# Optimization experiments

Hardware: AMD Instinct MI355X
Metric: run time of the kernel (lower is better)

## Reference

```python
import jax, jax.numpy as jnp
import numpy as np

B, N, D, H = 4, 2048, 512, 8
HD = D // H  # 64


def setup_inputs() -> dict:
    key = jax.random.key(0)
    ks = jax.random.split(key, 12)
    s = 0.02
    return {
        "x": jax.random.normal(ks[0], (B, N, D), jnp.float32),
        "freqs": jax.random.normal(ks[1], (B, N, HD // 2), jnp.float32),
        # weights stored as (in, out); torch Linear applies x @ W.T + b
        "wqkv_w": jax.random.normal(ks[2], (D, 3 * D), jnp.float32) * s,
        "wqkv_b": jax.random.normal(ks[3], (3 * D,), jnp.float32) * s,
        "out_w": jax.random.normal(ks[4], (D, D), jnp.float32) * s,
        "out_b": jax.random.normal(ks[5], (D,), jnp.float32) * s,
        "ffn1_w": jax.random.normal(ks[6], (2 * D, 2 * D), jnp.float32) * s,
        "ffn1_b": jax.random.normal(ks[7], (2 * D,), jnp.float32) * s,
        "ln_g": jnp.ones((2 * D,), jnp.float32),
        "ln_b": jnp.zeros((2 * D,), jnp.float32),
        "ffn2_w": jax.random.normal(ks[8], (2 * D, D), jnp.float32) * s,
        "ffn2_b": jax.random.normal(ks[9], (D,), jnp.float32) * s,
    }


def _rope(t, cos, sin):
    # t: [B,H,N,HD]; cos/sin: [B,1,N,HD/2]
    x1, x2 = t[..., ::2], t[..., 1::2]
    return jnp.stack([x1 * cos - x2 * sin, x1 * sin + x2 * cos], axis=-1).reshape(t.shape)


def reference(x, freqs, wqkv_w, wqkv_b, out_w, out_b,
              ffn1_w, ffn1_b, ln_g, ln_b, ffn2_w, ffn2_b):
    b, n, d = x.shape
    h, hd = H, d // H
    qkv = x @ wqkv_w + wqkv_b                      # [B,N,3D]
    q, k, v = jnp.split(qkv, 3, axis=-1)
    to_heads = lambda t: t.reshape(b, n, h, hd).transpose(0, 2, 1, 3)  # [B,H,N,HD]
    q, k, v = to_heads(q), to_heads(k), to_heads(v)
    cos = jnp.cos(freqs)[:, None]                  # [B,1,N,HD/2]
    sin = jnp.sin(freqs)[:, None]
    q = _rope(q, cos, sin)
    k = _rope(k, cos, sin)
    scale = hd ** -0.5
    attn = jax.nn.softmax(jnp.einsum('bhqd,bhkd->bhqk', q, k) * scale, axis=-1)
    msg = jnp.einsum('bhqk,bhkd->bhqd', attn, v).transpose(0, 2, 1, 3).reshape(b, n, d)
    msg = msg @ out_w + out_b
    # FFN on concat([x, msg]): Linear -> LayerNorm -> GELU(exact) -> Linear
    hcat = jnp.concatenate([x, msg], axis=-1) @ ffn1_w + ffn1_b   # [B,N,2D]
    mu = hcat.mean(-1, keepdims=True)
    var = hcat.var(-1, keepdims=True)
    hcat = (hcat - mu) * jax.lax.rsqrt(var + 1e-5) * ln_g + ln_b
    hcat = jax.nn.gelu(hcat, approximate=False)
    return x + hcat @ ffn2_w + ffn2_b
```

## Files before the change

### kernel.cpp

```cpp
#include <hip/hip_runtime.h>
#include <hip/hip_bf16.h>
#include <math.h>

typedef __bf16 bf16;
typedef __bf16 bf16x2 __attribute__((ext_vector_type(2)));
typedef __bf16 bf16x4 __attribute__((ext_vector_type(4)));
typedef __bf16 bf16x8 __attribute__((ext_vector_type(8)));
typedef float f32x4 __attribute__((ext_vector_type(4)));
typedef float f32x16 __attribute__((ext_vector_type(16)));

#define MFMA16(a, b, c) __builtin_amdgcn_mfma_f32_16x16x32_bf16(a, b, c, 0, 0, 0)
#define MFMA32(a, b, c) __builtin_amdgcn_mfma_f32_32x32x16_bf16(a, b, c, 0, 0, 0)


__global__ __launch_bounds__(256) void prep_kernel(
    const float* __restrict__ wqkv_w, const float* __restrict__ out_w,
    const float* __restrict__ ffn1_w, const float* __restrict__ ffn2_w,
    const float* __restrict__ x, const float* __restrict__ freqs,
    const float* __restrict__ ffn1_b, const float* __restrict__ out_b,
    bf16* __restrict__ wqkv_t, bf16* __restrict__ ffn2_t,
    bf16* __restrict__ fused_t, bf16* __restrict__ ffn1bt,
    bf16* __restrict__ out_cast, bf16* __restrict__ cat,
    float* __restrict__ bias_f, unsigned* __restrict__ tab)
{
    const int bid = blockIdx.x, tid = threadIdx.x;
    __shared__ bf16 tile[32][33];
    __shared__ float red[256];
    if (bid >= 6672) {
        int i = (bid - 6672) * 1024 + tid * 4;
        const float4 f = *(const float4*)(&freqs[i]);
        float s0, c0, s1, c1, s2, c2, s3, c3;
        __sincosf(f.x, &s0, &c0); __sincosf(f.y, &s1, &c1);
        __sincosf(f.z, &s2, &c2); __sincosf(f.w, &s3, &c3);
        union { bf16x2 h2; unsigned u; } p0, p1, p2, p3;
        p0.h2[0] = (bf16)c0; p0.h2[1] = (bf16)s0;
        p1.h2[0] = (bf16)c1; p1.h2[1] = (bf16)s1;
        p2.h2[0] = (bf16)c2; p2.h2[1] = (bf16)s2;
        p3.h2[0] = (bf16)c3; p3.h2[1] = (bf16)s3;
        uint4 o = {p0.u, p1.u, p2.u, p3.u};
        *(uint4*)(&tab[i]) = o;
        return;
    }
    if (bid >= 6656) {
        const int n = (bid - 6656) * 64 + (tid & 63);
        const int ic = tid >> 6;
        float acc = 0.f;
#pragma unroll 8
        for (int i = ic * 128; i < ic * 128 + 128; i++)
            acc += out_b[i] * ffn1_w[(size_t)(512 + i) * 1024 + n];
        red[tid] = acc;
        __syncthreads();
        if (tid < 64)
            bias_f[n] = ffn1_b[n] + red[tid] + red[tid + 64] + red[tid + 128] + red[tid + 192];
        return;
    }
    if (bid >= 2560) {
        int i = (bid - 2560) * 256 + tid;
        int row = i >> 7, col = (i & 127) << 2;
        const float4 v = *(const float4*)(&x[(size_t)row * 512 + col]);
        bf16x4 o; o[0] = (bf16)v.x; o[1] = (bf16)v.y; o[2] = (bf16)v.z; o[3] = (bf16)v.w;
        *(bf16x4*)(&cat[(size_t)row * 1024 + col]) = o;
        return;
    }
    if (bid >= 2304) {
        int i = (bid - 2304) * 1024 + tid * 4;
        const float4 v = *(const float4*)(&out_w[i]);
        bf16x4 o; o[0] = (bf16)v.x; o[1] = (bf16)v.y; o[2] = (bf16)v.z; o[3] = (bf16)v.w;
        *(bf16x4*)(&out_cast[i]) = o;
        return;
    }
    const float* src; bf16* dst; int C, ldd, bx, by;
    if (bid < 768)       { src = wqkv_w;            dst = wqkv_t;  C = 1536; ldd = 512;  int r = bid;        bx = r % 48; by = r / 48; }
    else if (bid < 1280) { src = ffn2_w;            dst = ffn2_t;  C = 512;  ldd = 1024; int r = bid - 768;  bx = r % 16; by = r / 16; }
    else if (bid < 1792) { src = ffn1_w;            dst = fused_t; C = 1024; ldd = 1024; int r = bid - 1280; bx = r % 32; by = r / 32; }
    else                 { src = ffn1_w + 512*1024; dst = ffn1bt;  C = 1024; ldd = 512;  int r = bid - 1792; bx = r % 32; by = r / 32; }
    const int tx = tid & 31, ty = tid >> 5;
    const int xx = bx * 32 + tx;
#pragma unroll
    for (int j = 0; j < 4; j++)
        tile[ty + 8 * j][tx] = (bf16)src[(size_t)(by * 32 + ty + 8 * j) * C + xx];
    __syncthreads();
    const int x2 = by * 32 + tx;
#pragma unroll
    for (int j = 0; j < 4; j++)
        dst[(size_t)(bx * 32 + ty + 8 * j) * ldd + x2] = tile[tx][ty + 8 * j];
}

__global__ __launch_bounds__(256) void qkv_wcomb_kernel(
    const bf16* __restrict__ cat, const bf16* __restrict__ wqkv_t,
    const float* __restrict__ wqkv_b, const unsigned* __restrict__ tab,
    bf16* __restrict__ qbuf, bf16* __restrict__ kbuf, bf16* __restrict__ vbuf,
    const bf16* __restrict__ ffn1bt, const bf16* __restrict__ out_cast,
    bf16* __restrict__ fused_t)
{
    const int bid = blockIdx.x;
    const bool isqkv = bid < 768;
    const bf16* A; const bf16* Bt; int lda, m0, n0;
    if (isqkv) { A = cat;    lda = 1024; Bt = wqkv_t;   n0 = (bid % 12) * 128; m0 = (bid / 12) * 128; }
    else       { int r = bid - 768;
                 A = ffn1bt; lda = 512;  Bt = out_cast; n0 = (r & 3) * 128;    m0 = (r >> 2) * 128; }
    const int K = 512;

    const int tid = threadIdx.x;
    const int lane = tid & 63, wave = tid >> 6;
    const int wm = wave >> 1, wn = wave & 1;
    const int l15 = lane & 15, quad = lane >> 4;

    __shared__ __align__(16) char smem[16384];
    bf16* As = (bf16*)smem;
    bf16* Bs = (bf16*)(smem + 8192);
    unsigned* tabs = (unsigned*)smem;

    const int c0 = tid, c1 = tid + 256;
    const int r0 = c0 >> 2, kc0 = (c0 & 3) << 3;
    const int r1 = c1 >> 2, kc1 = (c1 & 3) << 3;
    const bf16* pA0 = &A[(size_t)(m0 + r0) * lda + kc0];
    const bf16* pA1 = &A[(size_t)(m0 + r1) * lda + kc1];
    const bf16* pB0 = &Bt[(size_t)(n0 + r0) * K + kc0];
    const bf16* pB1 = &Bt[(size_t)(n0 + r1) * K + kc1];

    const f32x4 zero = {0.f, 0.f, 0.f, 0.f};
    f32x4 acc[4][4];
#pragma unroll
    for (int i = 0; i < 4; i++)
#pragma unroll
        for (int j = 0; j < 4; j++) acc[i][j] = zero;

    bf16x8 ra0 = *(const bf16x8*)pA0;
    bf16x8 ra1 = *(const bf16x8*)pA1;
    bf16x8 rb0 = *(const bf16x8*)pB0;
    bf16x8 rb1 = *(const bf16x8*)pB1;

    for (int k0 = 0; k0 < K; k0 += 32) {
        __syncthreads();
        *(bf16x8*)(&As[c0 * 8]) = ra0;
        *(bf16x8*)(&As[c1 * 8]) = ra1;
        *(bf16x8*)(&Bs[c0 * 8]) = rb0;
        *(bf16x8*)(&Bs[c1 * 8]) = rb1;
        __syncthreads();
        if (k0 + 32 < K) {
            ra0 = *(const bf16x8*)(pA0 + k0 + 32);
            ra1 = *(const bf16x8*)(pA1 + k0 + 32);
            rb0 = *(const bf16x8*)(pB0 + k0 + 32);
            rb1 = *(const bf16x8*)(pB1 + k0 + 32);
        }
        bf16x8 af[4], bfv[4];
#pragma unroll
        for (int t = 0; t < 4; t++) {
            af[t]  = *(const bf16x8*)(&As[(wm * 64 + t * 16 + l15) * 32 + quad * 8]);
            bfv[t] = *(const bf16x8*)(&Bs[(wn * 64 + t * 16 + l15) * 32 + quad * 8]);
        }
#pragma unroll
        for (int mt = 0; mt < 4; mt++)
#pragma unroll
            for (int nt = 0; nt < 4; nt++)
                acc[mt][nt] = MFMA16(af[mt], bfv[nt], acc[mt][nt]);
    }

    const int row_base = m0 + wm * 64;
    const int col_base = n0 + wn * 64;

    if (isqkv) {
        const int sector = col_base >> 9;
        const bool dorope = sector < 2;
        if (dorope) {
            __syncthreads();
#pragma unroll
            for (int ps = 0; ps < 4; ps++) {
                int idx = ps * 1024 + tid * 4;
                *(uint4*)(&tabs[idx]) = *(const uint4*)(&tab[(size_t)m0 * 32 + idx]);
            }
            __syncthreads();
        }
        const float SCQ = 0.125f * 1.44269504089f;
        bf16* dstbase = (sector == 0) ? qbuf : (sector == 1 ? kbuf : vbuf);
#pragma unroll
        for (int nt = 0; nt < 4; nt++) {
            const int col = col_base + nt * 16 + l15;
            const int cq = col & 511;
            const int h = cq >> 6, hd = cq & 63;
            const float bv = wqkv_b[col];
            const int ihalf = hd >> 1;
            const bool odd = (hd & 1) != 0;
#pragma unroll
            for (int mt = 0; mt < 4; mt++) {
#pragma unroll
                for (int r = 0; r < 4; r++) {
                    const int mrow = row_base + mt * 16 + quad * 4 + r;
                    float v = acc[mt][nt][r] + bv;
                    float o = v;
                    if (dorope) {
                        float p = __shfl_xor(v, 1);
                        const int rl = wm * 64 + mt * 16 + quad * 4 + r;
                        union { unsigned u; bf16x2 h2; } t2;
                        t2.u = tabs[rl * 32 + ihalf];
                        float cs = t2.h2[0], sn = t2.h2[1];
                        o = odd ? (p * sn + v * cs) : (v * cs - p * sn);
                        if (sector == 0) o *= SCQ;
                    }
                    const int b = mrow >> 11, n = mrow & 2047;
                    dstbase[(((size_t)b * 8 + h) * 2048 + n) * 64 + hd] = (bf16)o;
                }
            }
        }
    } else {
#pragma unroll
        for (int nt = 0; nt < 4; nt++) {
            const int col = col_base + nt * 16 + l15;
#pragma unroll
            for (int mt = 0; mt < 4; mt++) {
#pragma unroll
                for (int r = 0; r < 4; r++) {
                    const int row = row_base + mt * 16 + quad * 4 + r;
                    fused_t[(size_t)row * 1024 + 512 + col] = (bf16)acc[mt][nt][r];
                }
            }
        }
    }
}

template <int MODE>
__global__ __launch_bounds__(256) void gemm_mfma(
    const bf16* __restrict__ A, int lda, const bf16* __restrict__ Bt,
    const float* __restrict__ bias, void* __restrict__ outv,
    const float* __restrict__ auxf, int K)
{
    const int tid = threadIdx.x;
    const int lane = tid & 63, wave = tid >> 6;
    const int wm = wave >> 1, wn = wave & 1;
    const int l15 = lane & 15, quad = lane >> 4;
    const int m0 = blockIdx.y * 128;
    const int n0 = blockIdx.x * 128;

    __shared__ bf16 As[128 * 32];
    __shared__ bf16 Bs[128 * 32];

    const int c0 = tid, c1 = tid + 256;
    const int r0 = c0 >> 2, kc0 = (c0 & 3) << 3;
    const int r1 = c1 >> 2, kc1 = (c1 & 3) << 3;
    const bf16* pA0 = &A[(size_t)(m0 + r0) * lda + kc0];
    const bf16* pA1 = &A[(size_t)(m0 + r1) * lda + kc1];
    const bf16* pB0 = &Bt[(size_t)(n0 + r0) * K + kc0];
    const bf16* pB1 = &Bt[(size_t)(n0 + r1) * K + kc1];

    const f32x4 zero = {0.f, 0.f, 0.f, 0.f};
    f32x4 acc[4][4];
#pragma unroll
    for (int i = 0; i < 4; i++)
#pragma unroll
        for (int j = 0; j < 4; j++) acc[i][j] = zero;

    bf16x8 ra0 = *(const bf16x8*)pA0;
    bf16x8 ra1 = *(const bf16x8*)pA1;
    bf16x8 rb0 = *(const bf16x8*)pB0;
    bf16x8 rb1 = *(const bf16x8*)pB1;

    for (int k0 = 0; k0 < K; k0 += 32) {
        __syncthreads();
        *(bf16x8*)(&As[c0 * 8]) = ra0;
        *(bf16x8*)(&As[c1 * 8]) = ra1;
        *(bf16x8*)(&Bs[c0 * 8]) = rb0;
        *(bf16x8*)(&Bs[c1 * 8]) = rb1;
        __syncthreads();
        if (k0 + 32 < K) {
            ra0 = *(const bf16x8*)(pA0 + k0 + 32);
            ra1 = *(const bf16x8*)(pA1 + k0 + 32);
            rb0 = *(const bf16x8*)(pB0 + k0 + 32);
            rb1 = *(const bf16x8*)(pB1 + k0 + 32);
        }
        bf16x8 af[4], bfv[4];
#pragma unroll
        for (int t = 0; t < 4; t++) {
            af[t]  = *(const bf16x8*)(&As[(wm * 64 + t * 16 + l15) * 32 + quad * 8]);
            bfv[t] = *(const bf16x8*)(&Bs[(wn * 64 + t * 16 + l15) * 32 + quad * 8]);
        }
#pragma unroll
        for (int mt = 0; mt < 4; mt++)
#pragma unroll
            for (int nt = 0; nt < 4; nt++)
                acc[mt][nt] = MFMA16(af[mt], bfv[nt], acc[mt][nt]);
    }

    const int row_base = m0 + wm * 64;
    const int col_base = n0 + wn * 64;
#pragma unroll
    for (int nt = 0; nt < 4; nt++) {
        const int col = col_base + nt * 16 + l15;
        const float bv = bias[col];
#pragma unroll
        for (int mt = 0; mt < 4; mt++) {
#pragma unroll
            for (int r = 0; r < 4; r++) {
                const int row = row_base + mt * 16 + quad * 4 + r;
                float v = acc[mt][nt][r] + bv;
                if constexpr (MODE == 2) {
                    ((bf16*)outv)[(size_t)row * 1024 + col] = (bf16)v;
                } else {
                    v += auxf[(size_t)row * 512 + col];
                    ((float*)outv)[(size_t)row * 512 + col] = v;
                }
            }
        }
    }
}

__global__ __launch_bounds__(512) void attn_kernel(const bf16* __restrict__ qb,
                                                   const bf16* __restrict__ kb,
                                                   const bf16* __restrict__ vb,
                                                   bf16* __restrict__ cat)
{
    __shared__ __align__(16) char smem[35840];
    bf16* Ks  = (bf16*)smem;
    bf16* Vts = (bf16*)(smem + 128 * 72 * 2);

    const int tid = threadIdx.x, lane = tid & 63, wave = tid >> 6;
    const int l31 = lane & 31, half = lane >> 5;
    const int qg = wave >> 2, kh = wave & 3;
    const int bh = blockIdx.x >> 5, qt = blockIdx.x & 31;
    const int b = bh >> 3, h = bh & 7;
    const size_t base = (size_t)bh * 2048 * 64;
    const int m0 = qt * 64 + qg * 32;

    bf16x8 aq[4];
#pragma unroll
    for (int k4 = 0; k4 < 4; k4++)
        aq[k4] = *(const bf16x8*)(&qb[base + (size_t)(m0 + l31) * 64 + k4 * 16 + half * 8]);

    f32x16 accO[2];
#pragma unroll
    for (int i = 0; i < 16; i++) { accO[0][i] = 0.f; accO[1][i] = 0.f; }
    float lsum = 0.f;

    int krow[2], kcol[2];
#pragma unroll
    for (int i = 0; i < 2; i++) { int c = tid + i * 512; krow[i] = c >> 3; kcol[i] = (c & 7) << 3; }
    const int vpr = tid & 63, vdg = tid >> 6;

    bf16x8 kreg[2], vr0, vr1;
    auto prefetch = [&](int key0) {
#pragma unroll
        for (int i = 0; i < 2; i++)
            kreg[i] = *(const bf16x8*)(&kb[base + (size_t)(key0 + krow[i]) * 64 + kcol[i]]);
        vr0 = *(const bf16x8*)(&vb[base + (size_t)(key0 + 2 * vpr) * 64 + vdg * 8]);
        vr1 = *(const bf16x8*)(&vb[base + (size_t)(key0 + 2 * vpr + 1) * 64 + vdg * 8]);
    };

    prefetch(0);
    const int ko = kh * 32;
    for (int kt = 0; kt < 16; kt++) {
        __syncthreads();
#pragma unroll
        for (int i = 0; i < 2; i++)
            *(bf16x8*)(&Ks[krow[i] * 72 + kcol[i]]) = kreg[i];
#pragma unroll
        for (int j = 0; j < 8; j++) {
            bf16x2 pr; pr[0] = vr0[j]; pr[1] = vr1[j];
            *(bf16x2*)(&Vts[(vdg * 8 + j) * 136 + 2 * vpr]) = pr;
        }
        __syncthreads();
        if (kt < 15) prefetch((kt + 1) * 128);

        f32x16 s;
#pragma unroll
        for (int i = 0; i < 16; i++) s[i] = 0.f;
#pragma unroll
        for (int k4 = 0; k4 < 4; k4++) {
            bf16x8 ak = *(const bf16x8*)(&Ks[(ko + l31) * 72 + k4 * 16 + half * 8]);
            s = MFMA32(ak, aq[k4], s);
        }
        float p[16];
#pragma unroll
        for (int r = 0; r < 16; r++) p[r] = __builtin_amdgcn_exp2f(s[r]);
        lsum += (((p[0] + p[1]) + (p[2] + p[3])) + ((p[4] + p[5]) + (p[6] + p[7])))
              + (((p[8] + p[9]) + (p[10] + p[11])) + ((p[12] + p[13]) + (p[14] + p[15])));
        unsigned pk[8];
#pragma unroll
        for (int i2 = 0; i2 < 8; i2++) {
            union { bf16x2 hh; unsigned u; } t;
            t.hh[0] = (bf16)p[2 * i2]; t.hh[1] = (bf16)p[2 * i2 + 1];
            pk[i2] = t.u;
        }
        const unsigned sa = half ? pk[0] : pk[2];
        const unsigned sb = half ? pk[1] : pk[3];
        const unsigned sc2 = half ? pk[4] : pk[6];
        const unsigned sd = half ? pk[5] : pk[7];
        const unsigned ra = (unsigned)__shfl_xor((int)sa, 32);
        const unsigned rb = (unsigned)__shfl_xor((int)sb, 32);
        const unsigned rc = (unsigned)__shfl_xor((int)sc2, 32);
        const unsigned rd = (unsigned)__shfl_xor((int)sd, 32);
        union { bf16x8 v; unsigned u[4]; } B0, B1;
        B0.u[0] = half ? ra : pk[0];
        B0.u[1] = half ? rb : pk[1];
        B0.u[2] = half ? pk[2] : ra;
        B0.u[3] = half ? pk[3] : rb;
        B1.u[0] = half ? rc : pk[4];
        B1.u[1] = half ? rd : pk[5];
        B1.u[2] = half ? pk[6] : rc;
        B1.u[3] = half ? pk[7] : rd;
#pragma unroll
        for (int dh = 0; dh < 2; dh++) {
            bf16x8 av0 = *(const bf16x8*)(&Vts[(dh * 32 + l31) * 136 + ko + half * 8]);
            bf16x8 av1 = *(const bf16x8*)(&Vts[(dh * 32 + l31) * 136 + ko + 16 + half * 8]);
            accO[dh] = MFMA32(av0, B0.v, accO[dh]);
            accO[dh] = MFMA32(av1, B1.v, accO[dh]);
        }
    }

    auto slotp = [&](int s) { return (float*)smem + ((s * 2 + qg) * 64 + lane) * 33; };
    __syncthreads();
    if (kh == 1 || kh == 3) {
        float* pr2 = slotp(kh >> 1);
#pragma unroll
        for (int dh = 0; dh < 2; dh++)
#pragma unroll
            for (int r = 0; r < 16; r++) pr2[dh * 16 + r] = accO[dh][r];
        pr2[32] = lsum;
    }
    __syncthreads();
    if (kh == 0 || kh == 2) {
        float* pr2 = slotp(kh >> 1);
#pragma unroll
        for (int dh = 0; dh < 2; dh++)
#pragma unroll
            for (int r = 0; r < 16; r++) accO[dh][r] += pr2[dh * 16 + r];
        lsum += pr2[32];
    }
    __syncthreads();
    if (kh == 2) {
        float* pr2 = slotp(0);
#pragma unroll
        for (int dh = 0; dh < 2; dh++)
#pragma unroll
            for (int r = 0; r < 16; r++) pr2[dh * 16 + r] = accO[dh][r];
        pr2[32] = lsum;
    }
    __syncthreads();
    if (kh == 0) {
        float* pr2 = slotp(0);
#pragma unroll
        for (int dh = 0; dh < 2; dh++)
#pragma unroll
            for (int r = 0; r < 16; r++) accO[dh][r] += pr2[dh * 16 + r];
        lsum += pr2[32];
        lsum += __shfl_xor(lsum, 32);
        const float inv = 1.0f / lsum;
        const int n = m0 + l31;
        bf16* aor = cat + ((size_t)b * 2048 + n) * 1024 + 512 + h * 64;
#pragma unroll
        for (int dh = 0; dh < 2; dh++) {
#pragma unroll
            for (int g = 0; g < 4; g++) {
                bf16x4 o4;
#pragma unroll
                for (int e = 0; e < 4; e++) o4[e] = (bf16)(accO[dh][g * 4 + e] * inv);
                *(bf16x4*)(&aor[dh * 32 + g * 8 + half * 4]) = o4;
            }
        }
    }
}

__global__ __launch_bounds__(256) void ln_gelu_kernel(bf16* __restrict__ hb,
                                                      const float* __restrict__ g,
                                                      const float* __restrict__ bt)
{
    const int row = blockIdx.x, tid = threadIdx.x;
    const int lane = tid & 63, wave = tid >> 6;
    bf16* hr = hb + (size_t)row * 1024;
    bf16x4 hv = *(const bf16x4*)(&hr[tid * 4]);
    float v0 = hv[0], v1 = hv[1], v2 = hv[2], v3 = hv[3];
    float s = v0 + v1 + v2 + v3;
    float q = v0 * v0 + v1 * v1 + v2 * v2 + v3 * v3;
    for (int o = 32; o; o >>= 1) { s += __shfl_xor(s, o); q += __shfl_xor(q, o); }
    __shared__ float red[8];
    if (lane == 0) { red[wave] = s; red[4 + wave] = q; }
    __syncthreads();
    s = red[0] + red[1] + red[2] + red[3];
    q = red[4] + red[5] + red[6] + red[7];
    const float mu = s * (1.f / 1024.f);
    const float rstd = rsqrtf(q * (1.f / 1024.f) - mu * mu + 1e-5f);
    const float4 gv = *(const float4*)(&g[tid * 4]);
    const float4 bv = *(const float4*)(&bt[tid * 4]);
    float vv[4] = {v0, v1, v2, v3};
    const float gg[4] = {gv.x, gv.y, gv.z, gv.w};
    const float bb[4] = {bv.x, bv.y, bv.z, bv.w};
    bf16x4 o4;
#pragma unroll
    for (int i = 0; i < 4; i++) {
        float y = (vv[i] - mu) * rstd * gg[i] + bb[i];
        float t = 1.5957691216f * y * (1.0f + 0.044715f * y * y);
        float e = __builtin_amdgcn_exp2f(-1.44269504089f * t);
        o4[i] = (bf16)(y * __builtin_amdgcn_rcpf(1.0f + e));
    }
    *(bf16x4*)(&hr[tid * 4]) = o4;
}

extern "C" void kernel_launch(void* const* d_in, const int* in_sizes, int n_in,
                              void* d_out, int out_size, void* d_ws, size_t ws_size,
                              hipStream_t stream) {
    (void)in_sizes; (void)n_in; (void)out_size; (void)ws_size;
    const float* x      = (const float*)d_in[0];
    const float* freqs  = (const float*)d_in[1];
    const float* wqkv_w = (const float*)d_in[2];
    const float* wqkv_b = (const float*)d_in[3];
    const float* out_w  = (const float*)d_in[4];
    const float* out_b  = (const float*)d_in[5];
    const float* ffn1_w = (const float*)d_in[6];
    const float* ffn1_b = (const float*)d_in[7];
    const float* ln_g   = (const float*)d_in[8];
    const float* ln_b   = (const float*)d_in[9];
    const float* ffn2_w = (const float*)d_in[10];
    const float* ffn2_b = (const float*)d_in[11];
    float* out = (float*)d_out;
    bf16* ws   = (bf16*)d_ws;

    bf16* wqkv_t   = ws;
    bf16* ffn2_t   = wqkv_t + 1536 * 512;
    bf16* fused_t  = ffn2_t + 512 * 1024;
    bf16* ffn1bt   = fused_t + 1024 * 1024;
    bf16* out_cast = ffn1bt + 1024 * 512;
    bf16* cat      = out_cast + 512 * 512;
    bf16* qbuf     = cat + (size_t)8192 * 1024;
    bf16* kbuf     = qbuf + (size_t)8192 * 512;
    bf16* vbuf     = kbuf + (size_t)8192 * 512;
    float* bias_f  = (float*)(vbuf + (size_t)8192 * 512);
    unsigned* tab  = (unsigned*)(bias_f + 1024);
    bf16* hbuf     = qbuf;

    prep_kernel<<<6928, 256, 0, stream>>>(wqkv_w, out_w, ffn1_w, ffn2_w, x, freqs,
                                          ffn1_b, out_b,
                                          wqkv_t, ffn2_t, fused_t, ffn1bt, out_cast, cat,
                                          bias_f, tab);
    qkv_wcomb_kernel<<<800, 256, 0, stream>>>(cat, wqkv_t, wqkv_b, tab, qbuf, kbuf, vbuf,
                                              ffn1bt, out_cast, fused_t);
    attn_kernel<<<1024, 512, 0, stream>>>(qbuf, kbuf, vbuf, cat);
    gemm_mfma<2><<<dim3(8, 64), 256, 0, stream>>>(cat, 1024, fused_t, bias_f, hbuf, nullptr, 1024);
    ln_gelu_kernel<<<8192, 256, 0, stream>>>(hbuf, ln_g, ln_b);
    gemm_mfma<3><<<dim3(4, 64), 256, 0, stream>>>(hbuf, 1024, ffn2_t, ffn2_b, out, x, 1024);
}
```

Before: 256.4 us.

## Software-pipeline attention PV with double-buffered V tile and shrink GEMM N tiles

The attention kernel double-buffers the transposed V tile in shared memory and defers each tile's P·V MFMAs to the next iteration, so they issue alongside the next QK^T and exp work. This is meant to hide MFMA and exp latency, at the cost of more LDS per block (which may lower occupancy). Separately, the FFN GEMMs switch from 128x128 to 128x64 tiles, doubling the grid for better CU fill on the 256-CU part in exchange for less B-operand reuse per block.

```diff
diff --git a/kernel.cpp b/kernel.cpp
--- a/kernel.cpp
+++ b/kernel.cpp
@@ -220,75 +220,71 @@
 }
 
 template <int MODE>
-__global__ __launch_bounds__(256) void gemm_mfma(
+__global__ __launch_bounds__(256) void gemm64_mfma(
     const bf16* __restrict__ A, int lda, const bf16* __restrict__ Bt,
     const float* __restrict__ bias, void* __restrict__ outv,
     const float* __restrict__ auxf, int K)
 {
     const int tid = threadIdx.x;
     const int lane = tid & 63, wave = tid >> 6;
-    const int wm = wave >> 1, wn = wave & 1;
     const int l15 = lane & 15, quad = lane >> 4;
     const int m0 = blockIdx.y * 128;
-    const int n0 = blockIdx.x * 128;
+    const int n0 = blockIdx.x * 64;
 
     __shared__ bf16 As[128 * 32];
-    __shared__ bf16 Bs[128 * 32];
+    __shared__ bf16 Bs[64 * 32];
 
     const int c0 = tid, c1 = tid + 256;
-    const int r0 = c0 >> 2, kc0 = (c0 & 3) << 3;
-    const int r1 = c1 >> 2, kc1 = (c1 & 3) << 3;
-    const bf16* pA0 = &A[(size_t)(m0 + r0) * lda + kc0];
-    const bf16* pA1 = &A[(size_t)(m0 + r1) * lda + kc1];
-    const bf16* pB0 = &Bt[(size_t)(n0 + r0) * K + kc0];
-    const bf16* pB1 = &Bt[(size_t)(n0 + r1) * K + kc1];
+    const int ar0 = c0 >> 2, akc0 = (c0 & 3) << 3;
+    const int ar1 = c1 >> 2, akc1 = (c1 & 3) << 3;
+    const int br0 = tid >> 2, bkc0 = (tid & 3) << 3;
+    const bf16* pA0 = &A[(size_t)(m0 + ar0) * lda + akc0];
+    const bf16* pA1 = &A[(size_t)(m0 + ar1) * lda + akc1];
+    const bf16* pB0 = &Bt[(size_t)(n0 + br0) * K + bkc0];
 
     const f32x4 zero = {0.f, 0.f, 0.f, 0.f};
-    f32x4 acc[4][4];
-#pragma unroll
-    for (int i = 0; i < 4; i++)
+    f32x4 acc[2][4];
+#pragma unroll
+    for (int i = 0; i < 2; i++)
 #pragma unroll
         for (int j = 0; j < 4; j++) acc[i][j] = zero;
 
     bf16x8 ra0 = *(const bf16x8*)pA0;
     bf16x8 ra1 = *(const bf16x8*)pA1;
     bf16x8 rb0 = *(const bf16x8*)pB0;
-    bf16x8 rb1 = *(const bf16x8*)pB1;
 
     for (int k0 = 0; k0 < K; k0 += 32) {
         __syncthreads();
         *(bf16x8*)(&As[c0 * 8]) = ra0;
         *(bf16x8*)(&As[c1 * 8]) = ra1;
-        *(bf16x8*)(&Bs[c0 * 8]) = rb0;
-        *(bf16x8*)(&Bs[c1 * 8]) = rb1;
+        *(bf16x8*)(&Bs[tid * 8]) = rb0;
         __syncthreads();
         if (k0 + 32 < K) {
             ra0 = *(const bf16x8*)(pA0 + k0 + 32);
             ra1 = *(const bf16x8*)(pA1 + k0 + 32);
             rb0 = *(const bf16x8*)(pB0 + k0 + 32);
-            rb1 = *(const bf16x8*)(pB1 + k0 + 32);
-        }
-        bf16x8 af[4], bfv[4];
-#pragma unroll
-        for (int t = 0; t < 4; t++) {
-            af[t]  = *(const bf16x8*)(&As[(wm * 64 + t * 16 + l15) * 32 + quad * 8]);
-            bfv[t] = *(const bf16x8*)(&Bs[(wn * 64 + t * 16 + l15) * 32 + quad * 8]);
-        }
-#pragma unroll
-        for (int mt = 0; mt < 4; mt++)
+        }
+        bf16x8 af[2], bfv[4];
+#pragma unroll
+        for (int t = 0; t < 2; t++)
+            af[t] = *(const bf16x8*)(&As[(wave * 32 + t * 16 + l15) * 32 + quad * 8]);
+#pragma unroll
+        for (int t = 0; t < 4; t++)
+            bfv[t] = *(const bf16x8*)(&Bs[(t * 16 + l15) * 32 + quad * 8]);
+#pragma unroll
+        for (int mt = 0; mt < 2; mt++)
 #pragma unroll
             for (int nt = 0; nt < 4; nt++)
                 acc[mt][nt] = MFMA16(af[mt], bfv[nt], acc[mt][nt]);
     }
 
-    const int row_base = m0 + wm * 64;
-    const int col_base = n0 + wn * 64;
+    const int row_base = m0 + wave * 32;
 #pragma unroll
     for (int nt = 0; nt < 4; nt++) {
-        const int col = col_base + nt * 16 + l15;
+        const int col = n0 + nt * 16 + l15;
         const float bv = bias[col];
 #pragma unroll
-        for (int mt = 0; mt < 4; mt++) {
+        for (int mt = 0; mt < 2; mt++) {
 #pragma unroll
             for (int r = 0; r < 4; r++) {
                 const int row = row_base + mt * 16 + quad * 4 + r;
@@ -309,9 +305,10 @@
                                                    const bf16* __restrict__ vb,
                                                    bf16* __restrict__ cat)
 {
-    __shared__ __align__(16) char smem[35840];
-    bf16* Ks  = (bf16*)smem;
-    bf16* Vts = (bf16*)(smem + 128 * 72 * 2);
+    __shared__ __align__(16) char smem[53248];
+    bf16* Ks   = (bf16*)smem;
+    bf16* Vts0 = (bf16*)(smem + 18432);
+    bf16* Vts1 = (bf16*)(smem + 35840);
 
     const int tid = threadIdx.x, lane = tid & 63, wave = tid >> 6;
     const int l31 = lane & 31, half = lane >> 5;
@@ -345,9 +342,24 @@
         vr1 = *(const bf16x8*)(&vb[base + (size_t)(key0 + 2 * vpr + 1) * 64 + vdg * 8]);
     };
 
+    const int ko = kh * 32;
+    union Bu { bf16x8 v; unsigned u[4]; };
+    Bu B0p, B1p;
+    auto pv = [&](const bf16* Vr) {
+#pragma unroll
+        for (int dh = 0; dh < 2; dh++) {
+            bf16x8 av0 = *(const bf16x8*)(&Vr[(dh * 32 + l31) * 136 + ko + half * 8]);
+            bf16x8 av1 = *(const bf16x8*)(&Vr[(dh * 32 + l31) * 136 + ko + 16 + half * 8]);
+            accO[dh] = MFMA32(av0, B0p.v, accO[dh]);
+            accO[dh] = MFMA32(av1, B1p.v, accO[dh]);
+        }
+    };
+
     prefetch(0);
-    const int ko = kh * 32;
+#pragma unroll
     for (int kt = 0; kt < 16; kt++) {
+        bf16* Vw = (kt & 1) ? Vts1 : Vts0;
+        bf16* Vr = (kt & 1) ? Vts0 : Vts1;
         __syncthreads();
 #pragma unroll
         for (int i = 0; i < 2; i++)
@@ -355,7 +367,7 @@
 #pragma unroll
         for (int j = 0; j < 8; j++) {
             bf16x2 pr; pr[0] = vr0[j]; pr[1] = vr1[j];
-            *(bf16x2*)(&Vts[(vdg * 8 + j) * 136 + 2 * vpr]) = pr;
+            *(bf16x2*)(&Vw[(vdg * 8 + j) * 136 + 2 * vpr]) = pr;
         }
         __syncthreads();
         if (kt < 15) prefetch((kt + 1) * 128);
@@ -368,6 +380,7 @@
             bf16x8 ak = *(const bf16x8*)(&Ks[(ko + l31) * 72 + k4 * 16 + half * 8]);
             s = MFMA32(ak, aq[k4], s);
         }
+        if (kt > 0) pv(Vr);
         float p[16];
 #pragma unroll
         for (int r = 0; r < 16; r++) p[r] = __builtin_amdgcn_exp2f(s[r]);
@@ -388,25 +401,18 @@
         const unsigned rb = (unsigned)__shfl_xor((int)sb, 32);
         const unsigned rc = (unsigned)__shfl_xor((int)sc2, 32);
         const unsigned rd = (unsigned)__shfl_xor((int)sd, 32);
-        union { bf16x8 v; unsigned u[4]; } B0, B1;
-        B0.u[0] = half ? ra : pk[0];
-        B0.u[1] = half ? rb : pk[1];
-        B0.u[2] = half ? pk[2] : ra;
-        B0.u[3] = half ? pk[3] : rb;
-        B1.u[0] = half ? rc : pk[4];
-        B1.u[1] = half ? rd : pk[5];
-        B1.u[2] = half ? pk[6] : rc;
-        B1.u[3] = half ? pk[7] : rd;
-#pragma unroll
-        for (int dh = 0; dh < 2; dh++) {
-            bf16x8 av0 = *(const bf16x8*)(&Vts[(dh * 32 + l31) * 136 + ko + half * 8]);
-            bf16x8 av1 = *(const bf16x8*)(&Vts[(dh * 32 + l31) * 136 + ko + 16 + half * 8]);
-            accO[dh] = MFMA32(av0, B0.v, accO[dh]);
-            accO[dh] = MFMA32(av1, B1.v, accO[dh]);
-        }
-    }
-
-    auto slotp = [&](int s) { return (float*)smem + ((s * 2 + qg) * 64 + lane) * 33; };
+        B0p.u[0] = half ? ra : pk[0];
+        B0p.u[1] = half ? rb : pk[1];
+        B0p.u[2] = half ? pk[2] : ra;
+        B0p.u[3] = half ? pk[3] : rb;
+        B1p.u[0] = half ? rc : pk[4];
+        B1p.u[1] = half ? rd : pk[5];
+        B1p.u[2] = half ? pk[6] : rc;
+        B1p.u[3] = half ? pk[7] : rd;
+    }
+    pv(Vts1);
+
+    auto slotp = [&](int s2) { return (float*)smem + ((s2 * 2 + qg) * 64 + lane) * 33; };
     __syncthreads();
     if (kh == 1 || kh == 3) {
         float* pr2 = slotp(kh >> 1);
@@ -533,7 +539,7 @@
     qkv_wcomb_kernel<<<800, 256, 0, stream>>>(cat, wqkv_t, wqkv_b, tab, qbuf, kbuf, vbuf,
                                               ffn1bt, out_cast, fused_t);
     attn_kernel<<<1024, 512, 0, stream>>>(qbuf, kbuf, vbuf, cat);
-    gemm_mfma<2><<<dim3(8, 64), 256, 0, stream>>>(cat, 1024, fused_t, bias_f, hbuf, nullptr, 1024);
+    gemm64_mfma<2><<<dim3(16, 64), 256, 0, stream>>>(cat, 1024, fused_t, bias_f, hbuf, nullptr, 1024);
     ln_gelu_kernel<<<8192, 256, 0, stream>>>(hbuf, ln_g, ln_b);
-    gemm_mfma<3><<<dim3(4, 64), 256, 0, stream>>>(hbuf, 1024, ffn2_t, ffn2_b, out, x, 1024);
+    gemm64_mfma<3><<<dim3(8, 64), 256, 0, stream>>>(hbuf, 1024, ffn2_t, ffn2_b, out, x, 1024);
 }
```

Result: no change. 261.4 us (+2.0%).
